# Performance work log

Measured on AMD Instinct MI355X. Metric: run time of the kernel, lower is better.

Reference implementation:

```python
import jax, jax.numpy as jnp
import numpy as np

EMBED_DIM = 1024
NUM_HEADS = 16
HEAD_DIM = EMBED_DIM // NUM_HEADS
B, S = 4, 1024
EPS = 1e-5
NEG = -1e9


def layer_norm(h, gamma, beta):
    mu = jnp.mean(h, axis=-1, keepdims=True)
    var = jnp.mean(jnp.square(h - mu), axis=-1, keepdims=True)
    return (h - mu) * jax.lax.rsqrt(var + EPS) * gamma + beta


def setup_inputs() -> dict:
    key = jax.random.key(0)
    ks = jax.random.split(key, 8)
    scale = 1.0 / np.sqrt(EMBED_DIM)
    x = jax.random.normal(ks[0], (B, S, EMBED_DIM), dtype=jnp.float32)
    mask = jax.random.randint(ks[1], (B, S, S), 0, 2).astype(jnp.bool_)
    Wq = jax.random.uniform(ks[2], (EMBED_DIM, EMBED_DIM), jnp.float32, -scale, scale)
    bq = jax.random.uniform(ks[3], (EMBED_DIM,), jnp.float32, -scale, scale)
    Wk = jax.random.uniform(ks[4], (EMBED_DIM, EMBED_DIM), jnp.float32, -scale, scale)
    bk = jax.random.uniform(ks[5], (EMBED_DIM,), jnp.float32, -scale, scale)
    gq = jnp.ones((EMBED_DIM,), jnp.float32)
    bq_n = jnp.zeros((EMBED_DIM,), jnp.float32)
    gk = jnp.ones((EMBED_DIM,), jnp.float32)
    bk_n = jnp.zeros((EMBED_DIM,), jnp.float32)
    return {"x": x, "mask": mask, "Wq": Wq, "bq": bq, "Wk": Wk, "bk": bk,
            "gq": gq, "bq_n": bq_n, "gk": gk, "bk_n": bk_n}


def reference(x, mask, Wq, bq, Wk, bk, gq, bq_n, gk, bk_n):
    b, s, _ = x.shape
    # proj -> LayerNorm -> ReLU, split heads: [B,S,H,D]
    Q = jax.nn.relu(layer_norm(x @ Wq + bq, gq, bq_n)).reshape(b, s, NUM_HEADS, HEAD_DIM)
    K = jax.nn.relu(layer_norm(x @ Wk + bk, gk, bk_n)).reshape(b, s, NUM_HEADS, HEAD_DIM)
    # scores [B,H,S,S]
    scores = jnp.einsum('bqhd,bkhd->bhqk', Q, K) / np.sqrt(HEAD_DIM).astype(np.float32)
    # symmetric masking: mask applied along keys, then (via transpose trick) along queries
    m = (mask | jnp.swapaxes(mask, -1, -2))[:, None, :, :]
    scores = jnp.where(m, NEG, scores)
    attn = jax.nn.softmax(scores, axis=-1)
    return attn.mean(axis=1)  # [B,S,S]
```

## Files before the change

### kernel.cpp

```cpp
#include <hip/hip_runtime.h>
#include <hip/hip_bf16.h>

#define B_ 4
#define S_ 1024
#define E_ 1024
#define H_ 16
#define D_ 64

typedef __attribute__((ext_vector_type(8))) short short8;
typedef __attribute__((ext_vector_type(4))) float f32x4;

static __device__ __forceinline__ unsigned short f2bf(float x) {
  unsigned int u = __float_as_uint(x);
  unsigned int r = u + 0x7fffu + ((u >> 16) & 1u);
  return (unsigned short)(r >> 16);
}
static __device__ __forceinline__ float bf2f(unsigned short b) {
  return __uint_as_float((unsigned int)b << 16);
}

#define GL2LDS16(g, l)                                                            \
  __builtin_amdgcn_global_load_lds(                                               \
      (const __attribute__((address_space(1))) unsigned int*)(g),                 \
      (__attribute__((address_space(3))) unsigned int*)(l), 16, 0, 0)

__global__ __launch_bounds__(256) void prep_kernel(const int* __restrict__ mask,
                                                   const float* __restrict__ x,
                                                   const float* __restrict__ Wq,
                                                   const float* __restrict__ Wk,
                                                   unsigned char* __restrict__ msym,
                                                   unsigned short* __restrict__ xbf,
                                                   unsigned short* __restrict__ Wt) {
  __shared__ __align__(16) char u_lds[32 * 33 * 4];
  const int blk = blockIdx.x;
  const int tid = threadIdx.x;
  if (blk < 4096) {
    int (*T)[33] = (int(*)[33])u_lds;
    const int b = blk >> 10;
    const int rest = blk & 1023;
    const int i0 = (rest >> 5) << 5;
    const int j0 = (rest & 31) << 5;
    const int ii = tid >> 3;
    const int jj4 = (tid & 7) << 2;
    const size_t bO = (size_t)b * S_ * S_;
    const int4 m2 = *(const int4*)&mask[bO + (size_t)(j0 + ii) * S_ + i0 + jj4];
    T[ii][jj4 + 0] = m2.x; T[ii][jj4 + 1] = m2.y; T[ii][jj4 + 2] = m2.z; T[ii][jj4 + 3] = m2.w;
    __syncthreads();
    const int4 m1 = *(const int4*)&mask[bO + (size_t)(i0 + ii) * S_ + j0 + jj4];
    uchar4 o;
    o.x = ((m1.x != 0) || (T[jj4 + 0][ii] != 0)) ? 1 : 0;
    o.y = ((m1.y != 0) || (T[jj4 + 1][ii] != 0)) ? 1 : 0;
    o.z = ((m1.z != 0) || (T[jj4 + 2][ii] != 0)) ? 1 : 0;
    o.w = ((m1.w != 0) || (T[jj4 + 3][ii] != 0)) ? 1 : 0;
    *(uchar4*)&msym[bO + (size_t)(i0 + ii) * S_ + j0 + jj4] = o;
  } else if (blk < 6144) {
    const size_t i = ((size_t)(blk - 4096) * 256 + tid) * 8;
    const float4 a = *(const float4*)(x + i);
    const float4 b = *(const float4*)(x + i + 4);
    const ushort4 p0 = {f2bf(a.x), f2bf(a.y), f2bf(a.z), f2bf(a.w)};
    const ushort4 p1 = {f2bf(b.x), f2bf(b.y), f2bf(b.z), f2bf(b.w)};
    *(ushort4*)(xbf + i) = p0;
    *(ushort4*)(xbf + i + 4) = p1;
  } else {
    unsigned short (*T2)[36] = (unsigned short(*)[36])u_lds;
    const int wblk = blk - 6144;
    const int mat = wblk >> 10;
    const int kt = (wblk >> 5) & 31, ntb = wblk & 31;
    const float* W = mat ? Wk : Wq;
    const int r = tid >> 3, c4 = (tid & 7) << 2;
    const float4 v = *(const float4*)&W[(size_t)(kt * 32 + r) * 1024 + ntb * 32 + c4];
    T2[r][c4 + 0] = f2bf(v.x); T2[r][c4 + 1] = f2bf(v.y);
    T2[r][c4 + 2] = f2bf(v.z); T2[r][c4 + 3] = f2bf(v.w);
    __syncthreads();
    const ushort4 o = {T2[c4 + 0][r], T2[c4 + 1][r], T2[c4 + 2][r], T2[c4 + 3][r]};
    *(ushort4*)&Wt[(size_t)(mat * 1024 + ntb * 32 + r) * 1024 + kt * 32 + c4] = o;
  }
}

__global__ __launch_bounds__(256) void gemm_mfma_kernel(const unsigned short* __restrict__ Abf,
                                                        const unsigned short* __restrict__ Wt,
                                                        unsigned short* __restrict__ P,
                                                        int nstride) {
  __shared__ __align__(16) unsigned short As[128 * 32];
  __shared__ __align__(16) unsigned short Bs[128 * 32];
  const int tid = threadIdx.x;
  const int m0 = (blockIdx.x & 31) << 7;
  const int n0 = (blockIdx.x >> 5) << 7;
  const int wave = tid >> 6, lane = tid & 63;
  const int ln15 = lane & 15, rg = lane >> 4;
  const int wm = (wave & 1) << 6;
  const int wn = (wave >> 1) << 6;
  const int sr = tid >> 2;
  const int sc = (tid & 3) << 3;
  const unsigned short* gA = Abf + (size_t)(m0 + sr) * 1024 + sc;
  const unsigned short* gB = Wt + (size_t)(n0 + sr) * 1024 + sc;
  unsigned short* lA = As + tid * 8;
  unsigned short* lB = Bs + tid * 8;
  f32x4 acc[4][4];
#pragma unroll
  for (int i = 0; i < 4; ++i)
#pragma unroll
    for (int j = 0; j < 4; ++j) acc[i][j] = (f32x4){0.0f, 0.0f, 0.0f, 0.0f};

  const unsigned short* pa = As + (wm + ln15) * 32 + rg * 8;
  const unsigned short* pb = Bs + (wn + ln15) * 32 + rg * 8;
  for (int k0 = 0; k0 < E_; k0 += 32) {
    GL2LDS16(gA + k0, lA);
    GL2LDS16(gA + k0 + (size_t)64 * 1024, lA + 2048);
    GL2LDS16(gB + k0, lB);
    GL2LDS16(gB + k0 + (size_t)64 * 1024, lB + 2048);
    __syncthreads();
    short8 af[4], bfr[4];
#pragma unroll
    for (int i = 0; i < 4; ++i) af[i] = *(const short8*)(pa + i * 16 * 32);
#pragma unroll
    for (int j = 0; j < 4; ++j) bfr[j] = *(const short8*)(pb + j * 16 * 32);
#pragma unroll
    for (int i = 0; i < 4; ++i)
#pragma unroll
      for (int j = 0; j < 4; ++j)
        acc[i][j] = __builtin_amdgcn_mfma_f32_16x16x32_bf16(af[i], bfr[j], acc[i][j], 0, 0, 0);
    __syncthreads();
  }
#pragma unroll
  for (int i = 0; i < 4; ++i)
#pragma unroll
    for (int j = 0; j < 4; ++j)
#pragma unroll
      for (int r = 0; r < 4; ++r) {
        const int row = m0 + wm + i * 16 + rg * 4 + r;
        const int col = n0 + wn + j * 16 + ln15;
        P[(size_t)row * nstride + col] = f2bf(acc[i][j][r]);
      }
}

__device__ __forceinline__ void ln_body(const unsigned short* p, const float* bias,
                                        const float* gamma, const float* beta,
                                        unsigned short* obf, int b, int s, int tid) {
  const ushort4 pv = *(const ushort4*)(p + tid * 4);
  float4 v = {bf2f(pv.x), bf2f(pv.y), bf2f(pv.z), bf2f(pv.w)};
  const float4 bb = ((const float4*)bias)[tid];
  v.x += bb.x; v.y += bb.y; v.z += bb.z; v.w += bb.w;
  float sum = v.x + v.y + v.z + v.w;
  float s2 = v.x * v.x + v.y * v.y + v.z * v.z + v.w * v.w;
#pragma unroll
  for (int off = 32; off >= 1; off >>= 1) {
    sum += __shfl_xor(sum, off);
    s2 += __shfl_xor(s2, off);
  }
  __shared__ float red[2][4];
  const int wave = tid >> 6, lane = tid & 63;
  if (lane == 0) { red[0][wave] = sum; red[1][wave] = s2; }
  __syncthreads();
  sum = red[0][0] + red[0][1] + red[0][2] + red[0][3];
  s2 = red[1][0] + red[1][1] + red[1][2] + red[1][3];
  const float mu = sum * (1.0f / E_);
  const float var = s2 * (1.0f / E_) - mu * mu;
  const float r = rsqrtf(var + 1e-5f);
  const float4 g = ((const float4*)gamma)[tid];
  const float4 bt = ((const float4*)beta)[tid];
  const float o0 = fmaxf((v.x - mu) * r * g.x + bt.x, 0.0f);
  const float o1 = fmaxf((v.y - mu) * r * g.y + bt.y, 0.0f);
  const float o2 = fmaxf((v.z - mu) * r * g.z + bt.z, 0.0f);
  const float o3 = fmaxf((v.w - mu) * r * g.w + bt.w, 0.0f);
  const int h = tid >> 4;
  const int d = (tid & 15) << 2;
  const ushort4 ob = {f2bf(o0), f2bf(o1), f2bf(o2), f2bf(o3)};
  *(ushort4*)&obf[((size_t)(b * H_ + h) * S_ + s) * D_ + d] = ob;
}

__global__ __launch_bounds__(256) void ln_relu_bf_kernel(const unsigned short* __restrict__ P,
                                                         int rowstride, int coloff,
                                                         const float* __restrict__ bias,
                                                         const float* __restrict__ gamma,
                                                         const float* __restrict__ beta,
                                                         unsigned short* __restrict__ obf) {
  const int row = blockIdx.x;
  ln_body(P + (size_t)row * rowstride + coloff, bias, gamma, beta, obf,
          row >> 10, row & 1023, threadIdx.x);
}

__global__ __launch_bounds__(256) void ln2_kernel(const unsigned short* __restrict__ P2,
                                                  const float* __restrict__ bq,
                                                  const float* __restrict__ gq,
                                                  const float* __restrict__ bqn,
                                                  const float* __restrict__ bk,
                                                  const float* __restrict__ gk,
                                                  const float* __restrict__ bkn,
                                                  unsigned short* __restrict__ Qbf,
                                                  unsigned short* __restrict__ Kbf) {
  const int blk = blockIdx.x;
  const int sel = blk >> 12;
  const int row = blk & 4095;
  ln_body(P2 + (size_t)row * 2048 + sel * 1024,
          sel ? bk : bq, sel ? gk : gq, sel ? bkn : bqn,
          sel ? Kbf : Qbf, row >> 10, row & 1023, threadIdx.x);
}

__global__ __launch_bounds__(512, 4) void attn6_kernel(const unsigned short* __restrict__ Qbf,
                                                       const unsigned short* __restrict__ Kbf,
                                                       const unsigned char* __restrict__ msym,
                                                       float* __restrict__ out) {
  __shared__ __align__(16) unsigned short Qs[128 * 64];
  __shared__ __align__(16) unsigned short Ks[2][128 * 64];
  __shared__ __align__(16) float l_lds[16][8];
  const int tid = threadIdx.x;
  const int wave = tid >> 6, lane = tid & 63;
  const int ln15 = lane & 15, rg = lane >> 4;
  const int b = blockIdx.x & 3;
  const int hh = (blockIdx.x >> 2) & 1;
  const int q0 = (blockIdx.x >> 3) << 4;
  const unsigned short* Kb = Kbf + (size_t)(b * H_ + hh * 8) * S_ * D_;

  {
    const int rho = tid >> 2;
    const int c0 = (tid & 3) << 1;
    const int x = rho & 7;
    const unsigned short* src =
        Qbf + ((size_t)(b * H_ + hh * 8 + (rho >> 4)) * S_ + q0 + (rho & 15)) * D_ + c0 * 8;
    const uint4 v0 = *(const uint4*)src;
    const uint4 v1 = *(const uint4*)(src + 8);
    *(uint4*)&Qs[rho * 64 + (c0 ^ x) * 8] = v0;
    *(uint4*)&Qs[rho * 64 + ((c0 + 1) ^ x) * 8] = v1;
  }
  const int krow = tid >> 2, kc0 = (tid & 3) << 1;
  const int kx = krow & 7;
  const int kp0 = (kc0 ^ kx) * 8, kp1 = ((kc0 + 1) ^ kx) * 8;
  {
    const unsigned short* src = Kb + (size_t)krow * D_ + kc0 * 8;
    const uint4 p0 = *(const uint4*)src;
    const uint4 p1 = *(const uint4*)(src + 8);
    *(uint4*)&Ks[0][krow * 64 + kp0] = p0;
    *(uint4*)&Ks[0][krow * 64 + kp1] = p1;
  }
  unsigned int mbits = 0;
#pragma unroll
  for (int t = 0; t < 8; ++t)
#pragma unroll
    for (int r = 0; r < 4; ++r)
      mbits |= (msym[((size_t)b * S_ + q0 + rg * 4 + r) * S_ + t * 128 + wave * 16 + ln15] ? 1u : 0u)
               << (t * 4 + r);
  __syncthreads();

  const int pfrag = (rg ^ (ln15 & 7)) * 8;
  float o[8][4] = {};

#pragma unroll 1
  for (int hl = 0; hl < 8; ++hl) {
    const unsigned short* qrow = Qs + (hl * 16 + ln15) * 64;
    const short8 a0 = *(const short8*)(qrow + pfrag);
    const short8 a1 = *(const short8*)(qrow + (pfrag ^ 32));
    float la[4] = {0.0f, 0.0f, 0.0f, 0.0f};
    unsigned int epack[8][2];
#pragma unroll
    for (int t = 0; t < 8; ++t) {
      const bool more = (t < 7) || (hl < 7);
      uint4 pf0, pf1;
      if (more) {
        const int s1 = hl * 8 + t + 1;
        const unsigned short* src =
            Kb + ((size_t)(s1 >> 3) * S_ + ((s1 & 7) << 7) + krow) * D_ + kc0 * 8;
        pf0 = *(const uint4*)src;
        pf1 = *(const uint4*)(src + 8);
      }
      const unsigned short* kw = Ks[t & 1] + (wave * 16 + ln15) * 64;
      const short8 b0 = *(const short8*)(kw + pfrag);
      const short8 b1 = *(const short8*)(kw + (pfrag ^ 32));
      f32x4 cc = {0.0f, 0.0f, 0.0f, 0.0f};
      cc = __builtin_amdgcn_mfma_f32_16x16x32_bf16(a0, b0, cc, 0, 0, 0);
      cc = __builtin_amdgcn_mfma_f32_16x16x32_bf16(a1, b1, cc, 0, 0, 0);
      float e[4];
#pragma unroll
      for (int r = 0; r < 4; ++r) {
        const float sv = fminf(cc[r] * 0.125f, 80.0f);
        e[r] = ((mbits >> (t * 4 + r)) & 1u) ? 0.0f : __expf(sv);
        la[r] += e[r];
      }
      epack[t][0] = (unsigned)f2bf(e[0]) | ((unsigned)f2bf(e[1]) << 16);
      epack[t][1] = (unsigned)f2bf(e[2]) | ((unsigned)f2bf(e[3]) << 16);
      if (t == 7) {
#pragma unroll
        for (int r = 0; r < 4; ++r) {
          float lv = la[r];
          lv += __shfl_xor(lv, 1);
          lv += __shfl_xor(lv, 2);
          lv += __shfl_xor(lv, 4);
          lv += __shfl_xor(lv, 8);
          la[r] = lv;
        }
        if (ln15 == 0) {
#pragma unroll
          for (int r = 0; r < 4; ++r) l_lds[rg * 4 + r][wave] = la[r];
        }
      }
      if (more) {
        unsigned short* dst = Ks[(t + 1) & 1];
        *(uint4*)&dst[krow * 64 + kp0] = pf0;
        *(uint4*)&dst[krow * 64 + kp1] = pf1;
      }
      __syncthreads();
    }
#pragma unroll
    for (int r = 0; r < 4; ++r) {
      const float4 va = *(const float4*)&l_lds[rg * 4 + r][0];
      const float4 vb = *(const float4*)&l_lds[rg * 4 + r][4];
      const float ssum = ((va.x + va.y) + (va.z + va.w)) + ((vb.x + vb.y) + (vb.z + vb.w));
      const float li = 0.0625f * __builtin_amdgcn_rcpf(ssum);
#pragma unroll
      for (int t = 0; t < 8; ++t) {
        const unsigned u = epack[t][r >> 1];
        const float ev = (r & 1) ? __uint_as_float(u & 0xFFFF0000u) : __uint_as_float(u << 16);
        o[t][r] += ev * li;
      }
    }
  }
#pragma unroll
  for (int t = 0; t < 8; ++t)
#pragma unroll
    for (int r = 0; r < 4; ++r)
      atomicAdd(&out[((size_t)b * S_ + q0 + rg * 4 + r) * S_ + t * 128 + wave * 16 + ln15],
                o[t][r]);
}

extern "C" void kernel_launch(void* const* d_in, const int* in_sizes, int n_in,
                              void* d_out, int out_size, void* d_ws, size_t ws_size,
                              hipStream_t stream) {
  const float* x = (const float*)d_in[0];
  const int* mask = (const int*)d_in[1];
  const float* Wq = (const float*)d_in[2];
  const float* bq = (const float*)d_in[3];
  const float* Wk = (const float*)d_in[4];
  const float* bk = (const float*)d_in[5];
  const float* gq = (const float*)d_in[6];
  const float* bq_n = (const float*)d_in[7];
  const float* gk = (const float*)d_in[8];
  const float* bk_n = (const float*)d_in[9];
  float* out = (float*)d_out;

  char* ws = (char*)d_ws;
  const size_t MB = 1024 * 1024;

  if (ws_size >= 40 * MB) {
    unsigned short* P2 = (unsigned short*)ws;
    unsigned short* xbf = (unsigned short*)(ws + 16 * MB);
    unsigned short* Kbf = (unsigned short*)(ws + 16 * MB);
    unsigned short* Wt = (unsigned short*)(ws + 24 * MB);
    unsigned short* Qbf = (unsigned short*)(ws + 28 * MB);
    unsigned char* msym = (unsigned char*)(ws + 36 * MB);

    prep_kernel<<<8192, 256, 0, stream>>>(mask, x, Wq, Wk, msym, xbf, Wt);
    gemm_mfma_kernel<<<512, 256, 0, stream>>>(xbf, Wt, P2, 2048);
    ln2_kernel<<<8192, 256, 0, stream>>>(P2, bq, gq, bq_n, bk, gk, bk_n, Qbf, Kbf);
    hipMemsetAsync(out, 0, (size_t)B_ * S_ * S_ * sizeof(float), stream);
    attn6_kernel<<<512, 512, 0, stream>>>(Qbf, Kbf, msym, out);
  } else {
    unsigned short* P = (unsigned short*)ws;
    unsigned short* xbf = (unsigned short*)(ws + 8 * MB);
    unsigned short* Kbf = (unsigned short*)(ws + 8 * MB);
    unsigned short* Wt = (unsigned short*)(ws + 16 * MB);
    unsigned short* Qbf = (unsigned short*)(ws + 20 * MB);
    unsigned char* msym = (unsigned char*)(ws + 28 * MB);

    prep_kernel<<<8192, 256, 0, stream>>>(mask, x, Wq, Wk, msym, xbf, Wt);
    gemm_mfma_kernel<<<256, 256, 0, stream>>>(xbf, Wt, P, 1024);
    ln_relu_bf_kernel<<<4096, 256, 0, stream>>>(P, 1024, 0, bq, gq, bq_n, Qbf);
    gemm_mfma_kernel<<<256, 256, 0, stream>>>(xbf, Wt + (size_t)1024 * 1024, P, 1024);
    ln_relu_bf_kernel<<<4096, 256, 0, stream>>>(P, 1024, 0, bk, gk, bk_n, Kbf);
    hipMemsetAsync(out, 0, (size_t)B_ * S_ * S_ * sizeof(float), stream);
    attn6_kernel<<<512, 512, 0, stream>>>(Qbf, Kbf, msym, out);
  }
}
```

Before: 204.2 us.

## Give each attention block all 16 heads for 8 queries, drop memset and atomics

The attention kernel now assigns all 16 heads of 8 query rows to one block, so each block produces final output values and writes them with plain stores. This removes the output memset and the atomicAdd reduction across two head-halves. The 1/sqrt(D) scale is folded into the Q LayerNorm output, and K prefetch is deepened to two tiles ahead. The cost is that half of each MFMA's 16 rows are duplicate padding (rg>=2 lanes are wasted), so matmul work per useful output doubles, and the kernel reads more K data per block.

After: 413.5 us. 103% more time.

```diff
diff --git a/kernel.cpp b/kernel.cpp
--- a/kernel.cpp
+++ b/kernel.cpp
@@ -136,7 +136,8 @@
 
 __device__ __forceinline__ void ln_body(const unsigned short* p, const float* bias,
                                         const float* gamma, const float* beta,
-                                        unsigned short* obf, int b, int s, int tid) {
+                                        unsigned short* obf, int b, int s, int tid,
+                                        float oscale) {
   const ushort4 pv = *(const ushort4*)(p + tid * 4);
   float4 v = {bf2f(pv.x), bf2f(pv.y), bf2f(pv.z), bf2f(pv.w)};
   const float4 bb = ((const float4*)bias)[tid];
@@ -159,10 +160,10 @@
   const float r = rsqrtf(var + 1e-5f);
   const float4 g = ((const float4*)gamma)[tid];
   const float4 bt = ((const float4*)beta)[tid];
-  const float o0 = fmaxf((v.x - mu) * r * g.x + bt.x, 0.0f);
-  const float o1 = fmaxf((v.y - mu) * r * g.y + bt.y, 0.0f);
-  const float o2 = fmaxf((v.z - mu) * r * g.z + bt.z, 0.0f);
-  const float o3 = fmaxf((v.w - mu) * r * g.w + bt.w, 0.0f);
+  const float o0 = fmaxf((v.x - mu) * r * g.x + bt.x, 0.0f) * oscale;
+  const float o1 = fmaxf((v.y - mu) * r * g.y + bt.y, 0.0f) * oscale;
+  const float o2 = fmaxf((v.z - mu) * r * g.z + bt.z, 0.0f) * oscale;
+  const float o3 = fmaxf((v.w - mu) * r * g.w + bt.w, 0.0f) * oscale;
   const int h = tid >> 4;
   const int d = (tid & 15) << 2;
   const ushort4 ob = {f2bf(o0), f2bf(o1), f2bf(o2), f2bf(o3)};
@@ -174,10 +175,11 @@
                                                          const float* __restrict__ bias,
                                                          const float* __restrict__ gamma,
                                                          const float* __restrict__ beta,
-                                                         unsigned short* __restrict__ obf) {
+                                                         unsigned short* __restrict__ obf,
+                                                         float oscale) {
   const int row = blockIdx.x;
   ln_body(P + (size_t)row * rowstride + coloff, bias, gamma, beta, obf,
-          row >> 10, row & 1023, threadIdx.x);
+          row >> 10, row & 1023, threadIdx.x, oscale);
 }
 
 __global__ __launch_bounds__(256) void ln2_kernel(const unsigned short* __restrict__ P2,
@@ -194,10 +196,11 @@
   const int row = blk & 4095;
   ln_body(P2 + (size_t)row * 2048 + sel * 1024,
           sel ? bk : bq, sel ? gk : gq, sel ? bkn : bqn,
-          sel ? Kbf : Qbf, row >> 10, row & 1023, threadIdx.x);
-}
-
-__global__ __launch_bounds__(512, 4) void attn6_kernel(const unsigned short* __restrict__ Qbf,
+          sel ? Kbf : Qbf, row >> 10, row & 1023, threadIdx.x,
+          sel ? 1.0f : 0.125f);
+}
+
+__global__ __launch_bounds__(512, 4) void attn7_kernel(const unsigned short* __restrict__ Qbf,
                                                        const unsigned short* __restrict__ Kbf,
                                                        const unsigned char* __restrict__ msym,
                                                        float* __restrict__ out) {
@@ -208,16 +211,15 @@
   const int wave = tid >> 6, lane = tid & 63;
   const int ln15 = lane & 15, rg = lane >> 4;
   const int b = blockIdx.x & 3;
-  const int hh = (blockIdx.x >> 2) & 1;
-  const int q0 = (blockIdx.x >> 3) << 4;
-  const unsigned short* Kb = Kbf + (size_t)(b * H_ + hh * 8) * S_ * D_;
+  const int q0 = (blockIdx.x >> 2) << 3;
+  const unsigned short* Kb = Kbf + (size_t)b * H_ * S_ * D_;
 
   {
     const int rho = tid >> 2;
     const int c0 = (tid & 3) << 1;
     const int x = rho & 7;
     const unsigned short* src =
-        Qbf + ((size_t)(b * H_ + hh * 8 + (rho >> 4)) * S_ + q0 + (rho & 15)) * D_ + c0 * 8;
+        Qbf + ((size_t)(b * H_ + (rho >> 3)) * S_ + q0 + (rho & 7)) * D_ + c0 * 8;
     const uint4 v0 = *(const uint4*)src;
     const uint4 v1 = *(const uint4*)(src + 8);
     *(uint4*)&Qs[rho * 64 + (c0 ^ x) * 8] = v0;
@@ -226,42 +228,47 @@
   const int krow = tid >> 2, kc0 = (tid & 3) << 1;
   const int kx = krow & 7;
   const int kp0 = (kc0 ^ kx) * 8, kp1 = ((kc0 + 1) ^ kx) * 8;
+  unsigned int mbits = 0xFFFFFFFFu;
+  if (rg < 2) {
+    mbits = 0;
+#pragma unroll
+    for (int t = 0; t < 8; ++t)
+#pragma unroll
+      for (int r = 0; r < 4; ++r)
+        mbits |= (msym[((size_t)b * S_ + q0 + rg * 4 + r) * S_ + t * 128 + wave * 16 + ln15] ? 1u : 0u)
+                 << (t * 4 + r);
+  }
+  uint4 pf[2][2];
   {
-    const unsigned short* src = Kb + (size_t)krow * D_ + kc0 * 8;
-    const uint4 p0 = *(const uint4*)src;
-    const uint4 p1 = *(const uint4*)(src + 8);
-    *(uint4*)&Ks[0][krow * 64 + kp0] = p0;
-    *(uint4*)&Ks[0][krow * 64 + kp1] = p1;
-  }
-  unsigned int mbits = 0;
-#pragma unroll
-  for (int t = 0; t < 8; ++t)
-#pragma unroll
-    for (int r = 0; r < 4; ++r)
-      mbits |= (msym[((size_t)b * S_ + q0 + rg * 4 + r) * S_ + t * 128 + wave * 16 + ln15] ? 1u : 0u)
-               << (t * 4 + r);
+    const unsigned short* src0 = Kb + (size_t)krow * D_ + kc0 * 8;
+    pf[0][0] = *(const uint4*)src0;
+    pf[0][1] = *(const uint4*)(src0 + 8);
+    const unsigned short* src1 = src0 + (size_t)128 * D_;
+    pf[1][0] = *(const uint4*)src1;
+    pf[1][1] = *(const uint4*)(src1 + 8);
+    *(uint4*)&Ks[0][krow * 64 + kp0] = pf[0][0];
+    *(uint4*)&Ks[0][krow * 64 + kp1] = pf[0][1];
+  }
   __syncthreads();
 
   const int pfrag = (rg ^ (ln15 & 7)) * 8;
   float o[8][4] = {};
 
 #pragma unroll 1
-  for (int hl = 0; hl < 8; ++hl) {
-    const unsigned short* qrow = Qs + (hl * 16 + ln15) * 64;
+  for (int hl = 0; hl < 16; ++hl) {
+    const unsigned short* qrow = Qs + ((hl << 3) + (ln15 & 7)) * 64;
     const short8 a0 = *(const short8*)(qrow + pfrag);
     const short8 a1 = *(const short8*)(qrow + (pfrag ^ 32));
     float la[4] = {0.0f, 0.0f, 0.0f, 0.0f};
     unsigned int epack[8][2];
 #pragma unroll
     for (int t = 0; t < 8; ++t) {
-      const bool more = (t < 7) || (hl < 7);
-      uint4 pf0, pf1;
-      if (more) {
-        const int s1 = hl * 8 + t + 1;
+      if (hl < 15 || t < 6) {
+        const int s2 = hl * 8 + t + 2;
         const unsigned short* src =
-            Kb + ((size_t)(s1 >> 3) * S_ + ((s1 & 7) << 7) + krow) * D_ + kc0 * 8;
-        pf0 = *(const uint4*)src;
-        pf1 = *(const uint4*)(src + 8);
+            Kb + ((size_t)(s2 >> 3) * S_ + ((s2 & 7) << 7) + krow) * D_ + kc0 * 8;
+        pf[t & 1][0] = *(const uint4*)src;
+        pf[t & 1][1] = *(const uint4*)(src + 8);
       }
       const unsigned short* kw = Ks[t & 1] + (wave * 16 + ln15) * 64;
       const short8 b0 = *(const short8*)(kw + pfrag);
@@ -272,7 +279,7 @@
       float e[4];
 #pragma unroll
       for (int r = 0; r < 4; ++r) {
-        const float sv = fminf(cc[r] * 0.125f, 80.0f);
+        const float sv = fminf(cc[r], 80.0f);
         e[r] = ((mbits >> (t * 4 + r)) & 1u) ? 0.0f : __expf(sv);
         la[r] += e[r];
       }
@@ -293,10 +300,10 @@
           for (int r = 0; r < 4; ++r) l_lds[rg * 4 + r][wave] = la[r];
         }
       }
-      if (more) {
+      if (hl < 15 || t < 7) {
         unsigned short* dst = Ks[(t + 1) & 1];
-        *(uint4*)&dst[krow * 64 + kp0] = pf0;
-        *(uint4*)&dst[krow * 64 + kp1] = pf1;
+        *(uint4*)&dst[krow * 64 + kp0] = pf[(t + 1) & 1][0];
+        *(uint4*)&dst[krow * 64 + kp1] = pf[(t + 1) & 1][1];
       }
       __syncthreads();
     }
@@ -314,12 +321,13 @@
       }
     }
   }
-#pragma unroll
-  for (int t = 0; t < 8; ++t)
-#pragma unroll
-    for (int r = 0; r < 4; ++r)
-      atomicAdd(&out[((size_t)b * S_ + q0 + rg * 4 + r) * S_ + t * 128 + wave * 16 + ln15],
-                o[t][r]);
+  if (rg < 2) {
+#pragma unroll
+    for (int t = 0; t < 8; ++t)
+#pragma unroll
+      for (int r = 0; r < 4; ++r)
+        out[((size_t)b * S_ + q0 + rg * 4 + r) * S_ + t * 128 + wave * 16 + ln15] = o[t][r];
+  }
 }
 
 extern "C" void kernel_launch(void* const* d_in, const int* in_sizes, int n_in,
@@ -351,8 +359,7 @@
     prep_kernel<<<8192, 256, 0, stream>>>(mask, x, Wq, Wk, msym, xbf, Wt);
     gemm_mfma_kernel<<<512, 256, 0, stream>>>(xbf, Wt, P2, 2048);
     ln2_kernel<<<8192, 256, 0, stream>>>(P2, bq, gq, bq_n, bk, gk, bk_n, Qbf, Kbf);
-    hipMemsetAsync(out, 0, (size_t)B_ * S_ * S_ * sizeof(float), stream);
-    attn6_kernel<<<512, 512, 0, stream>>>(Qbf, Kbf, msym, out);
+    attn7_kernel<<<512, 512, 0, stream>>>(Qbf, Kbf, msym, out);
   } else {
     unsigned short* P = (unsigned short*)ws;
     unsigned short* xbf = (unsigned short*)(ws + 8 * MB);
@@ -363,10 +370,9 @@
 
     prep_kernel<<<8192, 256, 0, stream>>>(mask, x, Wq, Wk, msym, xbf, Wt);
     gemm_mfma_kernel<<<256, 256, 0, stream>>>(xbf, Wt, P, 1024);
-    ln_relu_bf_kernel<<<4096, 256, 0, stream>>>(P, 1024, 0, bq, gq, bq_n, Qbf);
+    ln_relu_bf_kernel<<<4096, 256, 0, stream>>>(P, 1024, 0, bq, gq, bq_n, Qbf, 0.125f);
     gemm_mfma_kernel<<<256, 256, 0, stream>>>(xbf, Wt + (size_t)1024 * 1024, P, 1024);
-    ln_relu_bf_kernel<<<4096, 256, 0, stream>>>(P, 1024, 0, bk, gk, bk_n, Kbf);
-    hipMemsetAsync(out, 0, (size_t)B_ * S_ * S_ * sizeof(float), stream);
-    attn6_kernel<<<512, 512, 0, stream>>>(Qbf, Kbf, msym, out);
-  }
-}
+    ln_relu_bf_kernel<<<4096, 256, 0, stream>>>(P, 1024, 0, bk, gk, bk_n, Kbf, 1.0f);
+    attn7_kernel<<<512, 512, 0, stream>>>(Qbf, Kbf, msym, out);
+  }
+}
```
